# Optimization experiments

Hardware: AMD Instinct MI355X
Metric: run time of the kernel (lower is better)

The kernel has to match this reference:

```python
import jax, jax.numpy as jnp
import numpy as np

D_MODEL = 1024
N_HEADS = 16
HEAD_DIM = D_MODEL // N_HEADS
CHUNK = 128
B, T = 2, 2048


def setup_inputs() -> dict:
    key = jax.random.key(0)
    ks = jax.random.split(key, 5)
    x = jax.random.normal(ks[0], (B, T, D_MODEL), dtype=jnp.float32)
    mk = lambda k: jax.random.normal(k, (D_MODEL, D_MODEL), dtype=jnp.float32) * 0.02
    return {"x": x, "Wq": mk(ks[1]), "Wk": mk(ks[2]), "Wv": mk(ks[3]), "Wo": mk(ks[4])}


def _chunked_causal_attention(q, k, v, cs):
    # q,k,v: [B,H,T,D] fp32. Streaming online-softmax over kv chunks (flash-attn style).
    Bq, H, Tq, D = q.shape
    n = Tq // cs  # T divisible by chunk_size
    inv_sqrt_d = 1.0 / (D ** 0.5)
    qc = jnp.moveaxis(q.reshape(Bq, H, n, cs, D), 2, 0)  # [n,B,H,cs,D]
    kc = jnp.moveaxis(k.reshape(Bq, H, n, cs, D), 2, 0)
    vc = jnp.moveaxis(v.reshape(Bq, H, n, cs, D), 2, 0)
    ar = jnp.arange(cs)

    def per_q(qi, qb):  # qb: [B,H,cs,D]
        q_idx = qi * cs + ar

        def step(carry, kv):
            m, l, o = carry
            ki, kb, vb = kv
            s = jnp.einsum('bhqd,bhkd->bhqk', qb, kb) * inv_sqrt_d
            k_idx = ki * cs + ar
            causal = q_idx[:, None] >= k_idx[None, :]
            s = jnp.where(causal, s, -jnp.inf)
            s_max = jnp.max(s, axis=-1, keepdims=True)
            m_new = jnp.maximum(m, s_max)
            # guard fully-masked chunks (m_new = -inf)
            m_safe = jnp.where(jnp.isneginf(m_new), 0.0, m_new)
            alpha = jnp.exp(m - m_safe)
            p = jnp.exp(s - m_safe)
            o = o * alpha + jnp.einsum('bhqk,bhkd->bhqd', p, vb)
            l = l * alpha + jnp.sum(p, axis=-1, keepdims=True)
            return (m_new, l, o), None

        init = (jnp.full((Bq, H, cs, 1), -jnp.inf, dtype=jnp.float32),
                jnp.zeros((Bq, H, cs, 1), dtype=jnp.float32),
                jnp.zeros_like(qb))
        (m, l, o), _ = jax.lax.scan(step, init, (jnp.arange(n), kc, vc))
        return o / jnp.maximum(l, 1e-9)

    out = jax.vmap(per_q)(jnp.arange(n), qc)  # [n,B,H,cs,D]
    return jnp.moveaxis(out, 0, 2).reshape(Bq, H, Tq, D)


def reference(x, Wq, Wk, Wv, Wo):
    Bx, Tx, C = x.shape
    def heads(w):
        return (x @ w.T).reshape(Bx, Tx, N_HEADS, HEAD_DIM).transpose(0, 2, 1, 3)
    q, k, v = heads(Wq), heads(Wk), heads(Wv)
    y = _chunked_causal_attention(q, k, v, CHUNK)  # [B,H,T,D]
    y = y.transpose(0, 2, 1, 3).reshape(Bx, Tx, C)
    return y @ Wo.T
```

## Files before the change

kernel.cpp:

```cpp
#include <hip/hip_runtime.h>
#include <hip/hip_bf16.h>
#include <stdint.h>

typedef __bf16 bf16;
typedef __bf16 bf16x8 __attribute__((ext_vector_type(8)));
typedef __bf16 bf16x4 __attribute__((ext_vector_type(4)));
typedef float  f32x4  __attribute__((ext_vector_type(4)));
typedef float  f32x16 __attribute__((ext_vector_type(16)));
typedef unsigned int u32;

#define DM 1024
#define NH 16
#define HD 64
#define TT 2048

#define QSCALE 0.18033688011112042f

__global__ void cvt_all(const float* __restrict__ x,  const float* __restrict__ wq,
                        const float* __restrict__ wk, const float* __restrict__ wv,
                        const float* __restrict__ wo,
                        bf16* __restrict__ xb,  bf16* __restrict__ wqb,
                        bf16* __restrict__ wkb, bf16* __restrict__ wvb,
                        bf16* __restrict__ wob) {
  const int i = (blockIdx.x * blockDim.x + threadIdx.x) * 4;
  const float* src; bf16* dst; int off;
  if (i < 4194304)      { src = x;  dst = xb;  off = i; }
  else {
    const int j = i - 4194304;
    const int w = j >> 20;
    off = j & 1048575;
    src = (w == 0) ? wq : (w == 1) ? wk : (w == 2) ? wv : wo;
    dst = (w == 0) ? wqb : (w == 1) ? wkb : (w == 2) ? wvb : wob;
  }
  const float4 v = *reinterpret_cast<const float4*>(src + off);
  bf16x4 o = { (bf16)v.x, (bf16)v.y, (bf16)v.z, (bf16)v.w };
  *reinterpret_cast<bf16x4*>(dst + off) = o;
}

static __device__ __forceinline__ void gload_lds16(const bf16* g, bf16* l) {
  __builtin_amdgcn_global_load_lds(
      (__attribute__((address_space(1))) void*)g,
      (__attribute__((address_space(3))) void*)l, 16, 0, 0);
}

static __device__ __forceinline__ int swzb(int lin) {
  return lin ^ (((lin >> 7) & 7) << 4);
}

static __device__ __forceinline__ u32 cvtpk(float lo, float hi) {
  u32 r;
  asm("v_cvt_pk_bf16_f32 %0, %1, %2" : "=v"(r) : "v"(lo), "v"(hi));
  return r;
}
static __device__ __forceinline__ void plswap(u32& a, u32& b) {
  asm("v_permlane32_swap_b32 %0, %1" : "+v"(a), "+v"(b));
}

__launch_bounds__(256, 3)
__global__ void gemm_qkv(const bf16* __restrict__ X, const bf16* __restrict__ Wq,
                         const bf16* __restrict__ Wk, const bf16* __restrict__ Wv,
                         bf16* __restrict__ Qb, bf16* __restrict__ Kb,
                         bf16* __restrict__ Vtb) {
  __shared__ bf16 As[128 * 32];
  __shared__ bf16 Bs[128 * 32];
  const int tid  = threadIdx.x;
  const int lane = tid & 63;
  const int wv   = tid >> 6;
  const int lg   = lane >> 4, lc = lane & 15;
  const int m0   = blockIdx.x * 128;
  const int ng   = blockIdx.y * 128;
  const int which = ng >> 10;
  const bf16* W = (which == 0) ? Wq : ((which == 1) ? Wk : Wv);
  const int n0 = ng & 1023;
  const int wm = wv >> 1, wn = wv & 1;

  f32x4 acc[4][4] = {};

  for (int k0 = 0; k0 < DM; k0 += 32) {
#pragma unroll
    for (int c = 0; c < 2; ++c) {
      const int e   = wv * 512 + c * 2048 + lane * 8;
      const int row = e >> 5, col = e & 31;
      gload_lds16(X + (size_t)(m0 + row) * DM + k0 + col, &As[wv * 512 + c * 2048]);
      gload_lds16(W + (size_t)(n0 + row) * DM + k0 + col, &Bs[wv * 512 + c * 2048]);
    }
    __syncthreads();
    bf16x8 a[4], b[4];
#pragma unroll
    for (int i = 0; i < 4; ++i)
      a[i] = *reinterpret_cast<const bf16x8*>(&As[(wm * 64 + i * 16 + lc) * 32 + lg * 8]);
#pragma unroll
    for (int j = 0; j < 4; ++j)
      b[j] = *reinterpret_cast<const bf16x8*>(&Bs[(wn * 64 + j * 16 + lc) * 32 + lg * 8]);
#pragma unroll
    for (int i = 0; i < 4; ++i)
#pragma unroll
      for (int j = 0; j < 4; ++j)
        acc[i][j] = __builtin_amdgcn_mfma_f32_16x16x32_bf16(a[i], b[j], acc[i][j], 0, 0, 0);
    __syncthreads();
  }

#pragma unroll
  for (int i = 0; i < 4; ++i) {
    const int mg = m0 + wm * 64 + i * 16 + lg * 4;
    const int bb = mg >> 11, t = mg & 2047;
#pragma unroll
    for (int j = 0; j < 4; ++j) {
      const int nl = n0 + wn * 64 + j * 16 + lc;
      const int h = nl >> 6, d = nl & 63;
      const int bh = bb * NH + h;
      const f32x4 v = acc[i][j];
      if (which == 0) {
        bf16* p = Qb + ((size_t)bh * TT + t) * HD + d;
#pragma unroll
        for (int r = 0; r < 4; ++r) p[r * HD] = (bf16)(v[r] * QSCALE);
      } else if (which == 1) {
        bf16* p = Kb + ((size_t)bh * TT + t) * HD + d;
#pragma unroll
        for (int r = 0; r < 4; ++r) p[r * HD] = (bf16)v[r];
      } else {
        bf16x4 pk = { (bf16)v[0], (bf16)v[1], (bf16)v[2], (bf16)v[3] };
        *reinterpret_cast<bf16x4*>(Vtb + ((size_t)bh * HD + d) * TT + t) = pk;
      }
    }
  }
}

#define MF32(a, b, c) __builtin_amdgcn_mfma_f32_32x32x16_bf16((a), (b), (c), 0, 0, 0)

__launch_bounds__(128, 2)
__global__ void attn_fwd(const bf16* __restrict__ Qb, const bf16* __restrict__ Kb,
                         const bf16* __restrict__ Vtb, bf16* __restrict__ Yb) {
  __shared__ bf16 Ks[2][4096];
  __shared__ bf16 Vs[2][4096];

  const int tid  = threadIdx.x;
  const int lane = tid & 63;
  const int wv   = tid >> 6;
  const int m31  = lane & 31;
  const int hi   = lane >> 5;
  const int hi16 = hi << 4;
  const int hi4  = hi << 2;
  const int xr   = (m31 & 7) << 4;
  const int kRow = m31 * 128;
  int colx[4];
#pragma unroll
  for (int i = 0; i < 4; ++i) colx[i] = (i * 32 + hi16) ^ xr;

  const int u    = blockIdx.x & 31;
  const int bh   = ((u & 7) << 2) | (u >> 3);
  const int qc   = 31 - (blockIdx.x >> 5);
  const int NT   = qc + 1;
  const int qb0  = qc * 64 + wv * 32;
  const int qrow = qb0 + m31;

  const bf16* Qg = Qb  + (size_t)bh * TT * HD;
  const bf16* Kg = Kb  + (size_t)bh * TT * HD;
  const bf16* Vg = Vtb + (size_t)bh * HD * TT;

  int dstb[4], koff[4], voff[4];
#pragma unroll
  for (int c = 0; c < 4; ++c) {
    const int base = (wv * 4 + c) * 1024;
    const int lin  = base + lane * 16;
    dstb[c] = base;
    koff[c] = swzb(lin);
    voff[c] = (lin >> 7) * (TT * 2) + (swzb(lin) & 127);
  }

  bf16x8 qr0 = *reinterpret_cast<const bf16x8*>(Qg + (size_t)qrow * HD + 0  + hi * 8);
  bf16x8 qr1 = *reinterpret_cast<const bf16x8*>(Qg + (size_t)qrow * HD + 16 + hi * 8);
  bf16x8 qr2 = *reinterpret_cast<const bf16x8*>(Qg + (size_t)qrow * HD + 32 + hi * 8);
  bf16x8 qr3 = *reinterpret_cast<const bf16x8*>(Qg + (size_t)qrow * HD + 48 + hi * 8);

  f32x16 o0 = {}, o1 = {};
  float m_run = -INFINITY, l_run = 0.f;

#define STAGE(buf, kv)                                                          \
  {                                                                             \
    _Pragma("unroll")                                                           \
    for (int c = 0; c < 4; ++c) {                                               \
      gload_lds16((const bf16*)((const char*)Kg + (size_t)(kv) * 8192 + koff[c]), \
                  (bf16*)((char*)Ks[buf] + dstb[c]));                           \
      gload_lds16((const bf16*)((const char*)Vg + (size_t)(kv) * 128 + voff[c]),  \
                  (bf16*)((char*)Vs[buf] + dstb[c]));                           \
    }                                                                           \
  }

  STAGE(0, 0);

  int cur = 0;
  for (int ti = 0; ti < NT; ++ti) {
    if (ti + 1 < NT) {
      STAGE(cur ^ 1, ti + 1);
      asm volatile("s_waitcnt vmcnt(8)" ::: "memory");
    } else {
      asm volatile("s_waitcnt vmcnt(0)" ::: "memory");
    }
    __builtin_amdgcn_s_barrier();
    __builtin_amdgcn_sched_barrier(0);

    const char* ksb = (const char*)Ks[cur];
    const char* vsb = (const char*)Vs[cur];
    const int k0 = ti * 64;

    f32x16 s0 = {}, s1 = {};
    __builtin_amdgcn_s_setprio(1);
    {
      bf16x8 kf;
      kf = *reinterpret_cast<const bf16x8*>(ksb + kRow + colx[0]); s0 = MF32(kf, qr0, s0);
      kf = *reinterpret_cast<const bf16x8*>(ksb + kRow + colx[1]); s0 = MF32(kf, qr1, s0);
      kf = *reinterpret_cast<const bf16x8*>(ksb + kRow + colx[2]); s0 = MF32(kf, qr2, s0);
      kf = *reinterpret_cast<const bf16x8*>(ksb + kRow + colx[3]); s0 = MF32(kf, qr3, s0);
      kf = *reinterpret_cast<const bf16x8*>(ksb + 4096 + kRow + colx[0]); s1 = MF32(kf, qr0, s1);
      kf = *reinterpret_cast<const bf16x8*>(ksb + 4096 + kRow + colx[1]); s1 = MF32(kf, qr1, s1);
      kf = *reinterpret_cast<const bf16x8*>(ksb + 4096 + kRow + colx[2]); s1 = MF32(kf, qr2, s1);
      kf = *reinterpret_cast<const bf16x8*>(ksb + 4096 + kRow + colx[3]); s1 = MF32(kf, qr3, s1);
    }
    __builtin_amdgcn_s_setprio(0);

    if (k0 + 63 > qb0) {
#pragma unroll
      for (int r = 0; r < 16; ++r) {
        const int kvl = (r & 3) + 8 * (r >> 2) + hi4;
        if (k0 + kvl > qrow)      s0[r] = -INFINITY;
        if (k0 + 32 + kvl > qrow) s1[r] = -INFINITY;
      }
    }

    float q0m = fmaxf(fmaxf(s0[0], s0[1]),  fmaxf(s0[2], s0[3]));
    float q1m = fmaxf(fmaxf(s0[4], s0[5]),  fmaxf(s0[6], s0[7]));
    float q2m = fmaxf(fmaxf(s0[8], s0[9]),  fmaxf(s0[10], s0[11]));
    float q3m = fmaxf(fmaxf(s0[12], s0[13]), fmaxf(s0[14], s0[15]));
    float q4m = fmaxf(fmaxf(s1[0], s1[1]),  fmaxf(s1[2], s1[3]));
    float q5m = fmaxf(fmaxf(s1[4], s1[5]),  fmaxf(s1[6], s1[7]));
    float q6m = fmaxf(fmaxf(s1[8], s1[9]),  fmaxf(s1[10], s1[11]));
    float q7m = fmaxf(fmaxf(s1[12], s1[13]), fmaxf(s1[14], s1[15]));
    float pm = fmaxf(fmaxf(fmaxf(q0m, q1m), fmaxf(q2m, q3m)),
                     fmaxf(fmaxf(q4m, q5m), fmaxf(q6m, q7m)));
    pm = fmaxf(pm, __shfl_xor(pm, 32));

    const int need = pm > m_run + 8.f;
    if (__any(need)) {
      const float mn = fmaxf(m_run, pm);
      const float al = __builtin_amdgcn_exp2f(m_run - mn);
      m_run = mn; l_run *= al;
#pragma unroll
      for (int r = 0; r < 16; ++r) { o0[r] *= al; o1[r] *= al; }
    }

#pragma unroll
    for (int r = 0; r < 16; ++r) {
      s0[r] = __builtin_amdgcn_exp2f(s0[r] - m_run);
      s1[r] = __builtin_amdgcn_exp2f(s1[r] - m_run);
    }

    union PU { u32 w[4]; bf16x8 v; } pu0, pu1, pu2, pu3;
    {
      u32 a0 = cvtpk(s0[0],  s0[1]),  a1 = cvtpk(s0[2],  s0[3]);
      u32 b0 = cvtpk(s0[4],  s0[5]),  b1 = cvtpk(s0[6],  s0[7]);
      plswap(a0, b0); plswap(a1, b1);
      pu0.w[0] = a0; pu0.w[1] = a1; pu0.w[2] = b0; pu0.w[3] = b1;
      u32 c0 = cvtpk(s0[8],  s0[9]),  c1 = cvtpk(s0[10], s0[11]);
      u32 d0 = cvtpk(s0[12], s0[13]), d1 = cvtpk(s0[14], s0[15]);
      plswap(c0, d0); plswap(c1, d1);
      pu1.w[0] = c0; pu1.w[1] = c1; pu1.w[2] = d0; pu1.w[3] = d1;
      u32 e0 = cvtpk(s1[0],  s1[1]),  e1 = cvtpk(s1[2],  s1[3]);
      u32 f0 = cvtpk(s1[4],  s1[5]),  f1 = cvtpk(s1[6],  s1[7]);
      plswap(e0, f0); plswap(e1, f1);
      pu2.w[0] = e0; pu2.w[1] = e1; pu2.w[2] = f0; pu2.w[3] = f1;
      u32 g0 = cvtpk(s1[8],  s1[9]),  g1 = cvtpk(s1[10], s1[11]);
      u32 h0 = cvtpk(s1[12], s1[13]), h1 = cvtpk(s1[14], s1[15]);
      plswap(g0, h0); plswap(g1, h1);
      pu3.w[0] = g0; pu3.w[1] = g1; pu3.w[2] = h0; pu3.w[3] = h1;
    }

    __builtin_amdgcn_s_setprio(1);
    {
      bf16x8 vf;
      vf = *reinterpret_cast<const bf16x8*>(vsb + kRow + colx[0]);        o0 = MF32(vf, pu0.v, o0);
      vf = *reinterpret_cast<const bf16x8*>(vsb + 4096 + kRow + colx[0]); o1 = MF32(vf, pu0.v, o1);
      vf = *reinterpret_cast<const bf16x8*>(vsb + kRow + colx[1]);        o0 = MF32(vf, pu1.v, o0);
      vf = *reinterpret_cast<const bf16x8*>(vsb + 4096 + kRow + colx[1]); o1 = MF32(vf, pu1.v, o1);
      vf = *reinterpret_cast<const bf16x8*>(vsb + kRow + colx[2]);        o0 = MF32(vf, pu2.v, o0);
      vf = *reinterpret_cast<const bf16x8*>(vsb + 4096 + kRow + colx[2]); o1 = MF32(vf, pu2.v, o1);
      vf = *reinterpret_cast<const bf16x8*>(vsb + kRow + colx[3]);        o0 = MF32(vf, pu3.v, o0);
      vf = *reinterpret_cast<const bf16x8*>(vsb + 4096 + kRow + colx[3]); o1 = MF32(vf, pu3.v, o1);
    }
    __builtin_amdgcn_s_setprio(0);

    float u0 = (s0[0] + s0[1]) + (s0[2] + s0[3]);
    float u1 = (s0[4] + s0[5]) + (s0[6] + s0[7]);
    float u2 = (s0[8] + s0[9]) + (s0[10] + s0[11]);
    float u3 = (s0[12] + s0[13]) + (s0[14] + s0[15]);
    float u4 = (s1[0] + s1[1]) + (s1[2] + s1[3]);
    float u5 = (s1[4] + s1[5]) + (s1[6] + s1[7]);
    float u6 = (s1[8] + s1[9]) + (s1[10] + s1[11]);
    float u7 = (s1[12] + s1[13]) + (s1[14] + s1[15]);
    float rsum = ((u0 + u1) + (u2 + u3)) + ((u4 + u5) + (u6 + u7));
    rsum += __shfl_xor(rsum, 32);
    l_run += rsum;

    __builtin_amdgcn_s_barrier();
    cur ^= 1;
  }
#undef STAGE

  {
    const float linv = 1.f / fmaxf(l_run, 1e-9f);
    bf16* yrow = Yb + ((size_t)((bh >> 4) * TT + qrow)) * DM + (bh & 15) * HD;
#pragma unroll
    for (int rq = 0; rq < 4; ++rq) {
      bf16x4 y0 = { (bf16)(o0[rq * 4 + 0] * linv), (bf16)(o0[rq * 4 + 1] * linv),
                    (bf16)(o0[rq * 4 + 2] * linv), (bf16)(o0[rq * 4 + 3] * linv) };
      *reinterpret_cast<bf16x4*>(yrow + rq * 8 + hi4) = y0;
      bf16x4 y1 = { (bf16)(o1[rq * 4 + 0] * linv), (bf16)(o1[rq * 4 + 1] * linv),
                    (bf16)(o1[rq * 4 + 2] * linv), (bf16)(o1[rq * 4 + 3] * linv) };
      *reinterpret_cast<bf16x4*>(yrow + 32 + rq * 8 + hi4) = y1;
    }
  }
}

__launch_bounds__(256, 2)
__global__ void gemm_out(const bf16* __restrict__ Y, const bf16* __restrict__ Wo,
                         float* __restrict__ Out) {
  __shared__ bf16 As[64 * 32];
  __shared__ bf16 Bs[128 * 32];
  const int tid  = threadIdx.x;
  const int lane = tid & 63;
  const int wv   = tid >> 6;
  const int lg   = lane >> 4, lc = lane & 15;
  const int m0   = blockIdx.x * 64;
  const int n0   = blockIdx.y * 128;
  const int wm = wv >> 1, wn = wv & 1;

  f32x4 acc[2][4] = {};

  for (int k0 = 0; k0 < DM; k0 += 32) {
    {
      const int e   = wv * 512 + lane * 8;
      const int row = e >> 5, col = e & 31;
      gload_lds16(Y + (size_t)(m0 + row) * DM + k0 + col, &As[wv * 512]);
    }
#pragma unroll
    for (int c = 0; c < 2; ++c) {
      const int e   = wv * 1024 + c * 512 + lane * 8;
      const int row = e >> 5, col = e & 31;
      gload_lds16(Wo + (size_t)(n0 + row) * DM + k0 + col, &Bs[wv * 1024 + c * 512]);
    }
    __syncthreads();
    bf16x8 a[2], b[4];
#pragma unroll
    for (int i = 0; i < 2; ++i)
      a[i] = *reinterpret_cast<const bf16x8*>(&As[(wm * 32 + i * 16 + lc) * 32 + lg * 8]);
#pragma unroll
    for (int j = 0; j < 4; ++j)
      b[j] = *reinterpret_cast<const bf16x8*>(&Bs[(wn * 64 + j * 16 + lc) * 32 + lg * 8]);
#pragma unroll
    for (int i = 0; i < 2; ++i)
#pragma unroll
      for (int j = 0; j < 4; ++j)
        acc[i][j] = __builtin_amdgcn_mfma_f32_16x16x32_bf16(a[i], b[j], acc[i][j], 0, 0, 0);
    __syncthreads();
  }

#pragma unroll
  for (int i = 0; i < 2; ++i) {
    const int mg = m0 + wm * 32 + i * 16 + lg * 4;
#pragma unroll
    for (int j = 0; j < 4; ++j) {
      const int n = n0 + wn * 64 + j * 16 + lc;
#pragma unroll
      for (int r = 0; r < 4; ++r)
        Out[(size_t)(mg + r) * DM + n] = acc[i][j][r];
    }
  }
}

extern "C" void kernel_launch(void* const* d_in, const int* in_sizes, int n_in,
                              void* d_out, int out_size, void* d_ws, size_t ws_size,
                              hipStream_t stream) {
  const float* x  = (const float*)d_in[0];
  const float* Wq = (const float*)d_in[1];
  const float* Wk = (const float*)d_in[2];
  const float* Wv = (const float*)d_in[3];
  const float* Wo = (const float*)d_in[4];
  float* out = (float*)d_out;
  char* ws = (char*)d_ws;
  const size_t MB = 1024 * 1024;

  bf16* xb  = (bf16*)(ws + 0);
  bf16* wqb = (bf16*)(ws + 8  * MB);
  bf16* wkb = (bf16*)(ws + 10 * MB);
  bf16* wvb = (bf16*)(ws + 12 * MB);
  bf16* wob = (bf16*)(ws + 14 * MB);
  bf16* Qb  = (bf16*)(ws + 16 * MB);
  bf16* Kb  = (bf16*)(ws + 24 * MB);
  bf16* Vtb = (bf16*)(ws + 32 * MB);
  bf16* yb  = xb;

  cvt_all<<<8192, 256, 0, stream>>>(x, Wq, Wk, Wv, Wo, xb, wqb, wkb, wvb, wob);
  gemm_qkv<<<dim3(32, 24), 256, 0, stream>>>(xb, wqb, wkb, wvb, Qb, Kb, Vtb);
  attn_fwd<<<1024, 128, 0, stream>>>(Qb, Kb, Vtb, yb);
  gemm_out<<<dim3(64, 8), 256, 0, stream>>>(yb, wob, out);
}
```

Before: 113.8 us.

## Double-buffer LDS tiles in projection GEMMs and reorder attention block scheduling

Both GEMM kernels now keep two LDS buffers and issue the next k-tile's global-to-LDS loads before computing on the current tile. Partial vmcnt waits and raw barriers let the copies overlap the MFMAs, and setprio raises wave priority during the MFMA burst. The attention kernel's block-to-query-chunk mapping changes from strictly longest-first to a grouped ordering that flips direction in the later groups, aiming to balance causal work across CUs. Double buffering doubles LDS use per block, and gemm_out's occupancy hint goes from 2 to 3, which may raise register pressure.

```diff
diff --git a/kernel.cpp b/kernel.cpp
--- a/kernel.cpp
+++ b/kernel.cpp
@@ -61,8 +61,8 @@
                          const bf16* __restrict__ Wk, const bf16* __restrict__ Wv,
                          bf16* __restrict__ Qb, bf16* __restrict__ Kb,
                          bf16* __restrict__ Vtb) {
-  __shared__ bf16 As[128 * 32];
-  __shared__ bf16 Bs[128 * 32];
+  __shared__ bf16 As[2][128 * 32];
+  __shared__ bf16 Bs[2][128 * 32];
   const int tid  = threadIdx.x;
   const int lane = tid & 63;
   const int wv   = tid >> 6;
@@ -74,31 +74,57 @@
   const int n0 = ng & 1023;
   const int wm = wv >> 1, wn = wv & 1;
 
+  int lrow[2], lcol[2], ldst[2];
+#pragma unroll
+  for (int c = 0; c < 2; ++c) {
+    const int e = wv * 512 + c * 2048 + lane * 8;
+    lrow[c] = e >> 5; lcol[c] = e & 31; ldst[c] = wv * 512 + c * 2048;
+  }
+
+#define QSTAGE(buf, kt)                                                        \
+  {                                                                            \
+    _Pragma("unroll")                                                          \
+    for (int c = 0; c < 2; ++c) {                                              \
+      gload_lds16(X + (size_t)(m0 + lrow[c]) * DM + (kt) * 32 + lcol[c],       \
+                  &As[buf][ldst[c]]);                                          \
+      gload_lds16(W + (size_t)(n0 + lrow[c]) * DM + (kt) * 32 + lcol[c],       \
+                  &Bs[buf][ldst[c]]);                                          \
+    }                                                                          \
+  }
+
   f32x4 acc[4][4] = {};
-
-  for (int k0 = 0; k0 < DM; k0 += 32) {
-#pragma unroll
-    for (int c = 0; c < 2; ++c) {
-      const int e   = wv * 512 + c * 2048 + lane * 8;
-      const int row = e >> 5, col = e & 31;
-      gload_lds16(X + (size_t)(m0 + row) * DM + k0 + col, &As[wv * 512 + c * 2048]);
-      gload_lds16(W + (size_t)(n0 + row) * DM + k0 + col, &Bs[wv * 512 + c * 2048]);
-    }
-    __syncthreads();
+  QSTAGE(0, 0);
+
+  int cur = 0;
+  for (int kt = 0; kt < 32; ++kt) {
+    if (kt + 1 < 32) {
+      QSTAGE(cur ^ 1, kt + 1);
+      asm volatile("s_waitcnt vmcnt(4)" ::: "memory");
+    } else {
+      asm volatile("s_waitcnt vmcnt(0)" ::: "memory");
+    }
+    __builtin_amdgcn_s_barrier();
+    __builtin_amdgcn_sched_barrier(0);
+
     bf16x8 a[4], b[4];
 #pragma unroll
     for (int i = 0; i < 4; ++i)
-      a[i] = *reinterpret_cast<const bf16x8*>(&As[(wm * 64 + i * 16 + lc) * 32 + lg * 8]);
+      a[i] = *reinterpret_cast<const bf16x8*>(&As[cur][(wm * 64 + i * 16 + lc) * 32 + lg * 8]);
 #pragma unroll
     for (int j = 0; j < 4; ++j)
-      b[j] = *reinterpret_cast<const bf16x8*>(&Bs[(wn * 64 + j * 16 + lc) * 32 + lg * 8]);
+      b[j] = *reinterpret_cast<const bf16x8*>(&Bs[cur][(wn * 64 + j * 16 + lc) * 32 + lg * 8]);
+    __builtin_amdgcn_s_setprio(1);
 #pragma unroll
     for (int i = 0; i < 4; ++i)
 #pragma unroll
       for (int j = 0; j < 4; ++j)
         acc[i][j] = __builtin_amdgcn_mfma_f32_16x16x32_bf16(a[i], b[j], acc[i][j], 0, 0, 0);
-    __syncthreads();
-  }
+    __builtin_amdgcn_s_setprio(0);
+
+    __builtin_amdgcn_s_barrier();
+    cur ^= 1;
+  }
+#undef QSTAGE
 
 #pragma unroll
   for (int i = 0; i < 4; ++i) {
@@ -149,7 +175,9 @@
 
   const int u    = blockIdx.x & 31;
   const int bh   = ((u & 7) << 2) | (u >> 3);
-  const int qc   = 31 - (blockIdx.x >> 5);
+  const int bhi  = blockIdx.x >> 8;
+  const int bmid = (blockIdx.x >> 5) & 7;
+  const int qc   = 8 * bhi + ((bhi < 2) ? bmid : (7 - bmid));
   const int NT   = qc + 1;
   const int qb0  = qc * 64 + wv * 32;
   const int qrow = qb0 + m31;
@@ -321,11 +349,11 @@
   }
 }
 
-__launch_bounds__(256, 2)
+__launch_bounds__(256, 3)
 __global__ void gemm_out(const bf16* __restrict__ Y, const bf16* __restrict__ Wo,
                          float* __restrict__ Out) {
-  __shared__ bf16 As[64 * 32];
-  __shared__ bf16 Bs[128 * 32];
+  __shared__ bf16 As[2][64 * 32];
+  __shared__ bf16 Bs[2][128 * 32];
   const int tid  = threadIdx.x;
   const int lane = tid & 63;
   const int wv   = tid >> 6;
@@ -334,35 +362,58 @@
   const int n0   = blockIdx.y * 128;
   const int wm = wv >> 1, wn = wv & 1;
 
+  const int ea   = wv * 512 + lane * 8;
+  const int arow = ea >> 5, acol = ea & 31, adst = wv * 512;
+  int brow[2], bcol[2], bdst[2];
+#pragma unroll
+  for (int c = 0; c < 2; ++c) {
+    const int e = wv * 1024 + c * 512 + lane * 8;
+    brow[c] = e >> 5; bcol[c] = e & 31; bdst[c] = wv * 1024 + c * 512;
+  }
+
+#define OSTAGE(buf, kt)                                                        \
+  {                                                                            \
+    gload_lds16(Y + (size_t)(m0 + arow) * DM + (kt) * 32 + acol,               \
+                &As[buf][adst]);                                               \
+    _Pragma("unroll")                                                          \
+    for (int c = 0; c < 2; ++c)                                                \
+      gload_lds16(Wo + (size_t)(n0 + brow[c]) * DM + (kt) * 32 + bcol[c],      \
+                  &Bs[buf][bdst[c]]);                                          \
+  }
+
   f32x4 acc[2][4] = {};
-
-  for (int k0 = 0; k0 < DM; k0 += 32) {
-    {
-      const int e   = wv * 512 + lane * 8;
-      const int row = e >> 5, col = e & 31;
-      gload_lds16(Y + (size_t)(m0 + row) * DM + k0 + col, &As[wv * 512]);
-    }
-#pragma unroll
-    for (int c = 0; c < 2; ++c) {
-      const int e   = wv * 1024 + c * 512 + lane * 8;
-      const int row = e >> 5, col = e & 31;
-      gload_lds16(Wo + (size_t)(n0 + row) * DM + k0 + col, &Bs[wv * 1024 + c * 512]);
-    }
-    __syncthreads();
+  OSTAGE(0, 0);
+
+  int cur = 0;
+  for (int kt = 0; kt < 32; ++kt) {
+    if (kt + 1 < 32) {
+      OSTAGE(cur ^ 1, kt + 1);
+      asm volatile("s_waitcnt vmcnt(3)" ::: "memory");
+    } else {
+      asm volatile("s_waitcnt vmcnt(0)" ::: "memory");
+    }
+    __builtin_amdgcn_s_barrier();
+    __builtin_amdgcn_sched_barrier(0);
+
     bf16x8 a[2], b[4];
 #pragma unroll
     for (int i = 0; i < 2; ++i)
-      a[i] = *reinterpret_cast<const bf16x8*>(&As[(wm * 32 + i * 16 + lc) * 32 + lg * 8]);
+      a[i] = *reinterpret_cast<const bf16x8*>(&As[cur][(wm * 32 + i * 16 + lc) * 32 + lg * 8]);
 #pragma unroll
     for (int j = 0; j < 4; ++j)
-      b[j] = *reinterpret_cast<const bf16x8*>(&Bs[(wn * 64 + j * 16 + lc) * 32 + lg * 8]);
+      b[j] = *reinterpret_cast<const bf16x8*>(&Bs[cur][(wn * 64 + j * 16 + lc) * 32 + lg * 8]);
+    __builtin_amdgcn_s_setprio(1);
 #pragma unroll
     for (int i = 0; i < 2; ++i)
 #pragma unroll
       for (int j = 0; j < 4; ++j)
         acc[i][j] = __builtin_amdgcn_mfma_f32_16x16x32_bf16(a[i], b[j], acc[i][j], 0, 0, 0);
-    __syncthreads();
-  }
+    __builtin_amdgcn_s_setprio(0);
+
+    __builtin_amdgcn_s_barrier();
+    cur ^= 1;
+  }
+#undef OSTAGE
 
 #pragma unroll
   for (int i = 0; i < 2; ++i) {
```

After: 115.0 us. About the same (+1.0%).
